# Performance work log

Hardware: AMD Instinct MI355X
Metric: run time of the kernel (lower is better)

The kernel has to match this reference:

```python
import jax, jax.numpy as jnp
import numpy as np

B, C, H, W = 8, 512, 64, 64
INTER = 64


def setup_inputs() -> dict:
    key = jax.random.key(0)
    ks = jax.random.split(key, 9)
    s_in = 1.0 / np.sqrt(C)
    return {
        "query": jax.random.normal(ks[0], (B, C, H, W), jnp.float32),
        "key_t": jax.random.normal(ks[1], (B, C, H, W), jnp.float32),
        "value": jax.random.normal(ks[2], (B, C, H, W), jnp.float32),
        # 1x1 conv weights (squeezed to [out, in]) and biases
        "Wq": jax.random.uniform(ks[3], (INTER, C), jnp.float32, -s_in, s_in),
        "bq": jax.random.uniform(ks[4], (INTER,), jnp.float32, -s_in, s_in),
        "Wk": jax.random.uniform(ks[5], (INTER, C), jnp.float32, -s_in, s_in),
        "bk": jax.random.uniform(ks[6], (INTER,), jnp.float32, -s_in, s_in),
        "Wv": jax.random.uniform(ks[7], (C, C), jnp.float32, -s_in, s_in),
        "bv": jax.random.uniform(ks[8], (C,), jnp.float32, -s_in, s_in),
        "gamma": jnp.full((1,), 0.5, jnp.float32),  # nonzero so attention path is exercised
    }


def reference(query, key_t, value, Wq, bq, Wk, bk, Wv, bv, gamma):
    # 1x1 convs = per-pixel channel matmuls
    pq = jnp.einsum('bchw,oc->bohw', query, Wq) + bq[None, :, None, None]   # [B,INTER,H,W]
    pk = jnp.einsum('bchw,oc->bohw', key_t, Wk) + bk[None, :, None, None]   # [B,INTER,H,W]
    pv = jnp.einsum('bchw,oc->bohw', value, Wv) + bv[None, :, None, None]   # [B,C,H,W]

    # column (height-axis) energies with -inf diagonal, row (width-axis) energies
    eH = jnp.einsum('bchw,bcgw->bhwg', pq, pk)                              # [B,H,W,H]
    eH = jnp.where(jnp.eye(H, dtype=bool)[:, None, :], -jnp.inf, eH)
    eW = jnp.einsum('bchw,bchf->bhwf', pq, pk)                              # [B,H,W,W]

    att = jax.nn.softmax(jnp.concatenate([eH, eW], axis=-1), axis=-1)      # [B,H,W,H+W]
    attH, attW = att[..., :H], att[..., H:]

    out = jnp.einsum('bcgw,bhwg->bchw', pv, attH) \
        + jnp.einsum('bchf,bhwf->bchw', pv, attW)
    return gamma[0] * out + value
```

## Files before the change

### kernel.cpp

```cpp
#include <hip/hip_runtime.h>
#include <hip/hip_bf16.h>

typedef __hip_bfloat16 bf16;
typedef __bf16 v8bf __attribute__((ext_vector_type(8)));
typedef float v4f __attribute__((ext_vector_type(4)));

#define NB 8
#define NC 512
#define NH 64
#define NW 64
#define NHW 4096
#define NI 64

__device__ __forceinline__ float b2f(bf16 x) { return __bfloat162float(x); }
__device__ __forceinline__ bf16  f2b(float x) { return __float2bfloat16(x); }

__global__ __launch_bounds__(256) void prep_kernel(const float* __restrict__ value,
                                                   const float* __restrict__ Wv,
                                                   bf16* __restrict__ vT,
                                                   bf16* __restrict__ Wb) {
  int t = threadIdx.x;
  if (blockIdx.x < 4096) {
    __shared__ float s[64][65];
    int i = blockIdx.x;
    int b = i >> 9, rem = i & 511;
    int c0 = (rem >> 6) * 64, px0 = (rem & 63) * 64;
    int lane = t & 63, row4 = t >> 6;
    const float* vp = value + (size_t)b * NC * NHW;
    for (int r = row4; r < 64; r += 4)
      s[r][lane] = vp[(size_t)(c0 + r) * NHW + px0 + lane];
    __syncthreads();
    bf16* op = vT + (size_t)b * NHW * NC;
    for (int r = row4; r < 64; r += 4)
      op[(size_t)(px0 + r) * NC + c0 + lane] = f2b(s[lane][r]);
  } else {
    size_t idx = (size_t)(blockIdx.x - 4096) * 1024 + t * 4;
    float4 w = *(const float4*)&Wv[idx];
    union { __bf16 h[4]; uint2 u; } pk;
    pk.h[0] = (__bf16)w.x; pk.h[1] = (__bf16)w.y;
    pk.h[2] = (__bf16)w.z; pk.h[3] = (__bf16)w.w;
    *(uint2*)&Wb[idx] = pk.u;
  }
}

__global__ __launch_bounds__(256) void gemm_nt(const bf16* __restrict__ Wb,
                                               const bf16* __restrict__ vT,
                                               const float* __restrict__ bias,
                                               bf16* __restrict__ out) {
  __shared__ __align__(16) __bf16 As[128 * 72];
  __shared__ __align__(16) __bf16 Bs[128 * 72];
  int t = threadIdx.x;
  int b = blockIdx.x >> 5, pxt = blockIdx.x & 31;
  int px0 = pxt * 128, o0 = blockIdx.y * 128;
  int wave = t >> 6, lane = t & 63;
  int wm = (wave >> 1) * 64, wn = (wave & 1) * 64;
  int row16 = lane & 15, quad = lane >> 4;
  v4f acc[4][4] = {};
  const bf16* Bp = vT + ((size_t)b * NHW + px0) * NC;
  for (int k0 = 0; k0 < NC; k0 += 64) {
#pragma unroll
    for (int ii = 0; ii < 4; ++ii) {
      int i = t + ii * 256;
      int m = i >> 3, ch = i & 7;
      *(uint4*)&As[m * 72 + ch * 8] = *(const uint4*)&Wb[(size_t)(o0 + m) * NC + k0 + ch * 8];
      *(uint4*)&Bs[m * 72 + ch * 8] = *(const uint4*)&Bp[(size_t)m * NC + k0 + ch * 8];
    }
    __syncthreads();
#pragma unroll
    for (int ks = 0; ks < 2; ++ks) {
      v8bf af[4], bf[4];
#pragma unroll
      for (int i = 0; i < 4; ++i) {
        af[i] = *(const v8bf*)&As[(wm + i * 16 + row16) * 72 + ks * 32 + quad * 8];
        bf[i] = *(const v8bf*)&Bs[(wn + i * 16 + row16) * 72 + ks * 32 + quad * 8];
      }
#pragma unroll
      for (int mi = 0; mi < 4; ++mi)
#pragma unroll
        for (int ni = 0; ni < 4; ++ni)
          acc[mi][ni] = __builtin_amdgcn_mfma_f32_16x16x32_bf16(af[mi], bf[ni],
                                                                acc[mi][ni], 0, 0, 0);
    }
    __syncthreads();
  }
#pragma unroll
  for (int mi = 0; mi < 4; ++mi)
#pragma unroll
    for (int r = 0; r < 4; ++r) {
      int m = wm + mi * 16 + quad * 4 + r;
      float bi = bias[o0 + m];
      bf16* orow = out + (size_t)(b * NC + o0 + m) * NHW + px0 + wn + row16;
#pragma unroll
      for (int ni = 0; ni < 4; ++ni)
        orow[ni * 16] = f2b(acc[mi][ni][r] + bi);
    }
}

__global__ __launch_bounds__(256) void proj64(const float* __restrict__ X0,
                                              const float* __restrict__ W0,
                                              const float* __restrict__ b0,
                                              bf16* __restrict__ o0p,
                                              const float* __restrict__ X1,
                                              const float* __restrict__ W1,
                                              const float* __restrict__ b1,
                                              bf16* __restrict__ o1p) {
  __shared__ __align__(16) __bf16 As[64 * 72];
  __shared__ __align__(16) __bf16 Bs[128 * 72];
  const float* X = (blockIdx.z == 0) ? X0 : X1;
  const float* Wm = (blockIdx.z == 0) ? W0 : W1;
  const float* bias = (blockIdx.z == 0) ? b0 : b1;
  bf16* out = (blockIdx.z == 0) ? o0p : o1p;
  int t = threadIdx.x;
  int b = blockIdx.x >> 5, nt = blockIdx.x & 31;
  int px0 = nt * 128;
  int wave = t >> 6, lane = t & 63;
  int wm = (wave >> 1) * 32, wn = (wave & 1) * 64;
  int row16 = lane & 15, quad = lane >> 4;
  v4f acc[2][4] = {};
  const float* Xb = X + (size_t)b * NC * NHW + px0;
  for (int k0 = 0; k0 < NC; k0 += 64) {
#pragma unroll
    for (int ii = 0; ii < 4; ++ii) {
      int f = t + ii * 256;
      int m = f >> 4, c4 = (f & 15) * 4;
      float4 w = *(const float4*)&Wm[(size_t)m * NC + k0 + c4];
      union { __bf16 h[4]; uint2 u; } pk;
      pk.h[0] = (__bf16)w.x; pk.h[1] = (__bf16)w.y;
      pk.h[2] = (__bf16)w.z; pk.h[3] = (__bf16)w.w;
      *(uint2*)&As[m * 72 + c4] = pk.u;
    }
#pragma unroll
    for (int r = 0; r < 2; ++r) {
      int idx = r * 256 + t;
      int ch4 = (idx >> 5) * 4, px4 = (idx & 31) * 4;
      float vv[4][4];
#pragma unroll
      for (int j = 0; j < 4; ++j)
        *(float4*)vv[j] = *(const float4*)&Xb[(size_t)(k0 + ch4 + j) * NHW + px4];
#pragma unroll
      for (int i = 0; i < 4; ++i) {
        union { __bf16 h[4]; uint2 u; } pk;
#pragma unroll
        for (int j = 0; j < 4; ++j) pk.h[j] = (__bf16)vv[j][i];
        int px = px4 + i;
        int boff = px * 144 + ((ch4 * 2) ^ (((px >> 2) & 7) << 4));
        *(uint2*)((char*)Bs + boff) = pk.u;
      }
    }
    __syncthreads();
#pragma unroll
    for (int ks = 0; ks < 2; ++ks) {
      v8bf af[2], bf[4];
#pragma unroll
      for (int i = 0; i < 2; ++i)
        af[i] = *(const v8bf*)&As[(wm + i * 16 + row16) * 72 + ks * 32 + quad * 8];
#pragma unroll
      for (int i = 0; i < 4; ++i) {
        int px = wn + i * 16 + row16;
        int boff = px * 144 + ((ks * 64 + quad * 16) ^ (((px >> 2) & 7) << 4));
        bf[i] = *(const v8bf*)((const char*)Bs + boff);
      }
#pragma unroll
      for (int mi = 0; mi < 2; ++mi)
#pragma unroll
        for (int ni = 0; ni < 4; ++ni)
          acc[mi][ni] = __builtin_amdgcn_mfma_f32_16x16x32_bf16(af[mi], bf[ni],
                                                                acc[mi][ni], 0, 0, 0);
    }
    __syncthreads();
  }
#pragma unroll
  for (int mi = 0; mi < 2; ++mi)
#pragma unroll
    for (int r = 0; r < 4; ++r) {
      int m = wm + mi * 16 + quad * 4 + r;
      float bi = bias[m];
      bf16* orow = out + (size_t)(b * NI + m) * NHW + px0 + wn + row16;
#pragma unroll
      for (int ni = 0; ni < 4; ++ni)
        orow[ni * 16] = f2b(acc[mi][ni][r] + bi);
    }
}

__device__ __forceinline__ void tile_mac(const float (*As)[68], const float (*Bs)[68],
                                         float acc[4][4], int tc, int tr) {
#pragma unroll 16
  for (int k = 0; k < 64; ++k) {
    float a0 = As[k][tc], a1 = As[k][tc + 1], a2 = As[k][tc + 2], a3 = As[k][tc + 3];
    float b0 = Bs[k][tr], b1 = Bs[k][tr + 1], b2 = Bs[k][tr + 2], b3 = Bs[k][tr + 3];
    acc[0][0] += a0 * b0; acc[0][1] += a0 * b1; acc[0][2] += a0 * b2; acc[0][3] += a0 * b3;
    acc[1][0] += a1 * b0; acc[1][1] += a1 * b1; acc[1][2] += a1 * b2; acc[1][3] += a1 * b3;
    acc[2][0] += a2 * b0; acc[2][1] += a2 * b1; acc[2][2] += a2 * b2; acc[2][3] += a2 * b3;
    acc[3][0] += a3 * b0; acc[3][1] += a3 * b1; acc[3][2] += a3 * b2; acc[3][3] += a3 * b3;
  }
}

__global__ __launch_bounds__(256) void score_kernel(const bf16* __restrict__ pq,
                                                    const bf16* __restrict__ pk,
                                                    float* __restrict__ att) {
  __shared__ float As[64][68];
  __shared__ float Bs[64][68];
  int t = threadIdx.x, lane = t & 63, row4 = t >> 6;
  int b = blockIdx.x >> 6, q = blockIdx.x & 63;
  bool isH = (blockIdx.y == 0);
  const bf16* pqb = pq + (size_t)b * NI * NHW;
  const bf16* pkb = pk + (size_t)b * NI * NHW;
  for (int o = row4; o < 64; o += 4) {
    size_t base = (size_t)o * NHW;
    if (isH) {
      As[o][lane] = b2f(pqb[base + (size_t)lane * NW + q]);
      Bs[o][lane] = b2f(pkb[base + (size_t)lane * NW + q]);
    } else {
      As[o][lane] = b2f(pqb[base + (size_t)q * NW + lane]);
      Bs[o][lane] = b2f(pkb[base + (size_t)q * NW + lane]);
    }
  }
  __syncthreads();
  int tc = (t & 15) * 4, tr = (t >> 4) * 4;
  float acc[4][4] = {};
  tile_mac(As, Bs, acc, tc, tr);
#pragma unroll
  for (int i = 0; i < 4; ++i)
#pragma unroll
    for (int j = 0; j < 4; ++j) {
      if (isH) {
        int h = tc + i, g = tr + j;
        float v = (h == g) ? -1e30f : acc[i][j];
        att[((size_t)(b * 64 + h) * 64 + q) * 128 + g] = v;
      } else {
        int w = tc + i, f = tr + j;
        att[((size_t)(b * 64 + q) * 64 + w) * 128 + 64 + f] = acc[i][j];
      }
    }
}

__global__ __launch_bounds__(256) void softmax_kernel(float* __restrict__ att) {
  int wave = threadIdx.x >> 6, lane = threadIdx.x & 63;
  int p = blockIdx.x * 4 + wave;
  float* row = att + (size_t)p * 128;
  float v0 = row[lane], v1 = row[lane + 64];
  float m = fmaxf(v0, v1);
#pragma unroll
  for (int off = 32; off; off >>= 1) m = fmaxf(m, __shfl_xor(m, off));
  float e0 = __expf(v0 - m), e1 = __expf(v1 - m);
  float s = e0 + e1;
#pragma unroll
  for (int off = 32; off; off >>= 1) s += __shfl_xor(s, off);
  float inv = 1.0f / s;
  bf16* rb = (bf16*)row;
  rb[lane] = f2b(e0 * inv);
  rb[lane + 64] = f2b(e1 * inv);
}

__global__ __launch_bounds__(256) void transpose_kernel(const bf16* __restrict__ in,
                                                        bf16* __restrict__ out) {
  __shared__ float s[64][65];
  int lane = threadIdx.x & 63, row4 = threadIdx.x >> 6;
  const bf16* ip = in + (size_t)blockIdx.x * 4096;
  bf16* op = out + (size_t)blockIdx.x * 4096;
  for (int r = row4; r < 64; r += 4) s[r][lane] = b2f(ip[r * 64 + lane]);
  __syncthreads();
  for (int r = row4; r < 64; r += 4) op[r * 64 + lane] = f2b(s[lane][r]);
}

__global__ __launch_bounds__(256) void apply_mfma(const bf16* pva,
                                                  const bf16* __restrict__ attb,
                                                  bf16* outp, int mode, int strided) {
  __shared__ __align__(16) __bf16 As[128 * 72];
  __shared__ __align__(16) __bf16 Bs[64 * 72];
  int t = threadIdx.x;
  int b = blockIdx.x >> 6, q = blockIdx.x & 63;
  int c0 = blockIdx.y * 128;
  int wave = t >> 6, lane = t & 63;
  int row16 = lane & 15, quad = lane >> 4;
#pragma unroll
  for (int ii = 0; ii < 4; ++ii) {
    int i = t + ii * 256;
    int m = i >> 3, ch = i & 7;
    if (!strided) {
      *(uint4*)&As[m * 72 + ch * 8] =
          *(const uint4*)&pva[((size_t)(b * NC + c0 + m) * 64 + q) * 64 + ch * 8];
    } else {
      union { __bf16 h[8]; uint4 u; } pk;
#pragma unroll
      for (int j = 0; j < 8; ++j)
        pk.h[j] = (__bf16)b2f(pva[(size_t)(b * NC + c0 + m) * 4096 +
                                  (size_t)(ch * 8 + j) * 64 + q]);
      *(uint4*)&As[m * 72 + ch * 8] = pk.u;
    }
  }
#pragma unroll
  for (int ii = 0; ii < 2; ++ii) {
    int i = t + ii * 256;
    int n = i >> 3, ch = i & 7;
    const bf16* src = (mode == 0)
        ? &attb[((size_t)(b * 64 + n) * 64 + q) * 256 + ch * 8]
        : &attb[((size_t)(b * 64 + q) * 64 + n) * 256 + 64 + ch * 8];
    *(uint4*)&Bs[n * 72 + ch * 8] = *(const uint4*)src;
  }
  __syncthreads();
  v4f acc[2][4] = {};
#pragma unroll
  for (int ks = 0; ks < 2; ++ks) {
    v8bf af[2], bfr[4];
#pragma unroll
    for (int mi = 0; mi < 2; ++mi)
      af[mi] = *(const v8bf*)&As[(wave * 32 + mi * 16 + row16) * 72 + ks * 32 + quad * 8];
#pragma unroll
    for (int ni = 0; ni < 4; ++ni)
      bfr[ni] = *(const v8bf*)&Bs[(ni * 16 + row16) * 72 + ks * 32 + quad * 8];
#pragma unroll
    for (int mi = 0; mi < 2; ++mi)
#pragma unroll
      for (int ni = 0; ni < 4; ++ni)
        acc[mi][ni] = __builtin_amdgcn_mfma_f32_16x16x32_bf16(af[mi], bfr[ni],
                                                              acc[mi][ni], 0, 0, 0);
  }
#pragma unroll
  for (int mi = 0; mi < 2; ++mi)
#pragma unroll
    for (int ni = 0; ni < 4; ++ni)
#pragma unroll
      for (int r = 0; r < 4; ++r) {
        int c = c0 + wave * 32 + mi * 16 + quad * 4 + r;
        int hw = row16 + ni * 16;
        outp[((size_t)(b * NC + c) * 64 + q) * 64 + hw] = f2b(acc[mi][ni][r]);
      }
}

__global__ __launch_bounds__(256) void combine_kernel(const bf16* __restrict__ t1,
                                                      const bf16* t2,
                                                      const float* __restrict__ value,
                                                      const float* __restrict__ gamma,
                                                      float* __restrict__ out) {
  __shared__ float s[64][65];
  int lane = threadIdx.x & 63, row4 = threadIdx.x >> 6;
  size_t bc = blockIdx.x;
  const bf16* t1p = t1 + bc * 4096;
  for (int r = row4; r < 64; r += 4) s[r][lane] = b2f(t1p[r * 64 + lane]);
  __syncthreads();
  float g = gamma[0];
  const bf16* t2p = t2 + bc * 4096;
  const float* vp = value + bc * 4096;
  float* op = out + bc * 4096;
  for (int r = row4; r < 64; r += 4)
    op[r * 64 + lane] = g * (s[lane][r] + b2f(t2p[r * 64 + lane])) + vp[r * 64 + lane];
}

extern "C" void kernel_launch(void* const* d_in, const int* in_sizes, int n_in,
                              void* d_out, int out_size, void* d_ws, size_t ws_size,
                              hipStream_t stream) {
  const float* query = (const float*)d_in[0];
  const float* key_t = (const float*)d_in[1];
  const float* value = (const float*)d_in[2];
  const float* Wq    = (const float*)d_in[3];
  const float* bq    = (const float*)d_in[4];
  const float* Wk    = (const float*)d_in[5];
  const float* bk    = (const float*)d_in[6];
  const float* Wv    = (const float*)d_in[7];
  const float* bv    = (const float*)d_in[8];
  const float* gamma = (const float*)d_in[9];
  float* out = (float*)d_out;

  char* ws = (char*)d_ws;
  bool full = ws_size >= (120ull << 20);
  bf16*  pq  = (bf16*)(ws);
  bf16*  Wb  = (bf16*)(ws);
  bf16*  pk  = (bf16*)(ws + (4ull << 20));
  float* att = (float*)(ws + (8ull << 20));
  bf16*  attb = (bf16*)att;
  bf16*  pv  = (bf16*)(ws + (24ull << 20));
  bf16*  pvT = (bf16*)(ws + (56ull << 20));
  bf16*  vT  = (bf16*)(ws + ((full ? 88ull : 56ull) << 20));
  bf16*  t1  = vT;
  bf16*  t2  = pv;

  dim3 blk(256);
  prep_kernel<<<4096 + 256, blk, 0, stream>>>(value, Wv, vT, Wb);
  gemm_nt<<<dim3(NB * 32, 4), blk, 0, stream>>>(Wb, vT, bv, pv);
  if (full) transpose_kernel<<<NB * NC, blk, 0, stream>>>(pv, pvT);
  proj64<<<dim3(NB * 32, 1, 2), blk, 0, stream>>>(
      query, Wq, bq, pq, key_t, Wk, bk, pk);
  score_kernel<<<dim3(NB * 64, 2), blk, 0, stream>>>(pq, pk, att);
  softmax_kernel<<<NB * NHW / 4, blk, 0, stream>>>(att);
  apply_mfma<<<dim3(NB * 64, 4), blk, 0, stream>>>(
      full ? pvT : pv, attb, t1, 0, full ? 0 : 1);
  apply_mfma<<<dim3(NB * 64, 4), blk, 0, stream>>>(pv, attb, t2, 1, 0);
  combine_kernel<<<NB * NC, blk, 0, stream>>>(t1, t2, value, gamma, out);
}
```

Before: 365.3 us.

## Double-buffer projection input via direct global-to-LDS loads, pre-convert Wq/Wk

Replaces the Q/K 1x1-conv projection kernel with one that streams fp32 activation tiles straight into LDS using global_load_lds, double-buffered so the next channel slice loads while MFMAs run on the current one. The LDS layout uses a rotated column swizzle to reduce bank conflicts. Wq and Wk are now converted to bf16 once in the prep kernel and read directly from global memory as MFMA A-fragments, instead of being converted and staged per block. Values are converted fp32->bf16 when read from LDS, which adds scalar LDS reads and conversions. The extra weight buffer reuses workspace space later overwritten by the attention scores.

```diff
diff --git a/kernel.cpp b/kernel.cpp
--- a/kernel.cpp
+++ b/kernel.cpp
@@ -17,8 +17,12 @@
 
 __global__ __launch_bounds__(256) void prep_kernel(const float* __restrict__ value,
                                                    const float* __restrict__ Wv,
+                                                   const float* __restrict__ Wq,
+                                                   const float* __restrict__ Wk,
                                                    bf16* __restrict__ vT,
-                                                   bf16* __restrict__ Wb) {
+                                                   bf16* __restrict__ Wb,
+                                                   bf16* __restrict__ Wqb,
+                                                   bf16* __restrict__ Wkb) {
   int t = threadIdx.x;
   if (blockIdx.x < 4096) {
     __shared__ float s[64][65];
@@ -34,12 +38,17 @@
     for (int r = row4; r < 64; r += 4)
       op[(size_t)(px0 + r) * NC + c0 + lane] = f2b(s[lane][r]);
   } else {
-    size_t idx = (size_t)(blockIdx.x - 4096) * 1024 + t * 4;
-    float4 w = *(const float4*)&Wv[idx];
+    int wb = blockIdx.x - 4096;
+    const float* src; bf16* dst; int lb;
+    if (wb < 256)      { src = Wv; dst = Wb;  lb = wb; }
+    else if (wb < 288) { src = Wq; dst = Wqb; lb = wb - 256; }
+    else               { src = Wk; dst = Wkb; lb = wb - 288; }
+    size_t idx = (size_t)lb * 1024 + t * 4;
+    float4 w = *(const float4*)&src[idx];
     union { __bf16 h[4]; uint2 u; } pk;
     pk.h[0] = (__bf16)w.x; pk.h[1] = (__bf16)w.y;
     pk.h[2] = (__bf16)w.z; pk.h[3] = (__bf16)w.w;
-    *(uint2*)&Wb[idx] = pk.u;
+    *(uint2*)&dst[idx] = pk.u;
   }
 }
 
@@ -96,78 +105,91 @@
     }
 }
 
-__global__ __launch_bounds__(256) void proj64(const float* __restrict__ X0,
-                                              const float* __restrict__ W0,
-                                              const float* __restrict__ b0,
-                                              bf16* __restrict__ o0p,
-                                              const float* __restrict__ X1,
-                                              const float* __restrict__ W1,
-                                              const float* __restrict__ b1,
-                                              bf16* __restrict__ o1p) {
-  __shared__ __align__(16) __bf16 As[64 * 72];
-  __shared__ __align__(16) __bf16 Bs[128 * 72];
-  const float* X = (blockIdx.z == 0) ? X0 : X1;
-  const float* Wm = (blockIdx.z == 0) ? W0 : W1;
+__global__ __launch_bounds__(256) void proj_lds(const float* __restrict__ X0,
+                                                const bf16* __restrict__ Wb0,
+                                                const float* __restrict__ b0,
+                                                bf16* __restrict__ o0p,
+                                                const float* __restrict__ X1,
+                                                const bf16* __restrict__ Wb1,
+                                                const float* __restrict__ b1,
+                                                bf16* __restrict__ o1p) {
+  __shared__ __align__(16) float Xs[2][64][128];
+  const float* X    = (blockIdx.z == 0) ? X0 : X1;
+  const bf16*  Wmb  = (blockIdx.z == 0) ? Wb0 : Wb1;
   const float* bias = (blockIdx.z == 0) ? b0 : b1;
-  bf16* out = (blockIdx.z == 0) ? o0p : o1p;
+  bf16* out         = (blockIdx.z == 0) ? o0p : o1p;
   int t = threadIdx.x;
   int b = blockIdx.x >> 5, nt = blockIdx.x & 31;
   int px0 = nt * 128;
   int wave = t >> 6, lane = t & 63;
   int wm = (wave >> 1) * 32, wn = (wave & 1) * 64;
   int row16 = lane & 15, quad = lane >> 4;
+  const float* Xb = X + (size_t)b * NC * NHW + px0;
+  int lhalf = lane >> 5;
+  int lcol  = (lane & 31) << 4;
   v4f acc[2][4] = {};
-  const float* Xb = X + (size_t)b * NC * NHW + px0;
-  for (int k0 = 0; k0 < NC; k0 += 64) {
-#pragma unroll
-    for (int ii = 0; ii < 4; ++ii) {
-      int f = t + ii * 256;
-      int m = f >> 4, c4 = (f & 15) * 4;
-      float4 w = *(const float4*)&Wm[(size_t)m * NC + k0 + c4];
-      union { __bf16 h[4]; uint2 u; } pk;
-      pk.h[0] = (__bf16)w.x; pk.h[1] = (__bf16)w.y;
-      pk.h[2] = (__bf16)w.z; pk.h[3] = (__bf16)w.w;
-      *(uint2*)&As[m * 72 + c4] = pk.u;
-    }
-#pragma unroll
-    for (int r = 0; r < 2; ++r) {
-      int idx = r * 256 + t;
-      int ch4 = (idx >> 5) * 4, px4 = (idx & 31) * 4;
-      float vv[4][4];
-#pragma unroll
-      for (int j = 0; j < 4; ++j)
-        *(float4*)vv[j] = *(const float4*)&Xb[(size_t)(k0 + ch4 + j) * NHW + px4];
-#pragma unroll
-      for (int i = 0; i < 4; ++i) {
-        union { __bf16 h[4]; uint2 u; } pk;
-#pragma unroll
-        for (int j = 0; j < 4; ++j) pk.h[j] = (__bf16)vv[j][i];
-        int px = px4 + i;
-        int boff = px * 144 + ((ch4 * 2) ^ (((px >> 2) & 7) << 4));
-        *(uint2*)((char*)Bs + boff) = pk.u;
+#pragma unroll
+  for (int i = 0; i < 8; ++i) {
+    int c  = (wave << 4) + (i << 1);
+    int ch = c + lhalf;
+    int pxl = ((lcol - (((ch >> 3) & 7) << 6)) & 511) >> 2;
+    const float* g = Xb + (size_t)ch * NHW + pxl;
+    __builtin_amdgcn_global_load_lds(
+        (const __attribute__((address_space(1))) void*)g,
+        (__attribute__((address_space(3))) void*)&Xs[0][c][0], 16, 0, 0);
+  }
+#pragma unroll
+  for (int k = 0; k < 8; ++k) {
+    int k0 = k * 64;
+    v8bf af[2][2];
+#pragma unroll
+    for (int ks = 0; ks < 2; ++ks)
+#pragma unroll
+      for (int i = 0; i < 2; ++i)
+        af[ks][i] = *(const v8bf*)&Wmb[(size_t)(wm + i * 16 + row16) * NC +
+                                       k0 + ks * 32 + quad * 8];
+    __builtin_amdgcn_sched_barrier(0);
+    if (k != 7) {
+      int kn = k0 + 64;
+#pragma unroll
+      for (int i = 0; i < 8; ++i) {
+        int c  = (wave << 4) + (i << 1);
+        int ch = c + lhalf;
+        int pxl = ((lcol - (((ch >> 3) & 7) << 6)) & 511) >> 2;
+        const float* g = Xb + (size_t)(kn + ch) * NHW + pxl;
+        __builtin_amdgcn_global_load_lds(
+            (const __attribute__((address_space(1))) void*)g,
+            (__attribute__((address_space(3))) void*)&Xs[(k + 1) & 1][c][0], 16, 0, 0);
       }
-    }
-    __syncthreads();
+      asm volatile("s_waitcnt vmcnt(8)" ::: "memory");
+    } else {
+      asm volatile("s_waitcnt vmcnt(0)" ::: "memory");
+    }
+    __builtin_amdgcn_s_barrier();
+    const float(*Xc)[128] = Xs[k & 1];
 #pragma unroll
     for (int ks = 0; ks < 2; ++ks) {
-      v8bf af[2], bf[4];
-#pragma unroll
-      for (int i = 0; i < 2; ++i)
-        af[i] = *(const v8bf*)&As[(wm + i * 16 + row16) * 72 + ks * 32 + quad * 8];
+      int rot = (ks * 4 + quad) << 6;
+      v8bf bfr[4];
 #pragma unroll
       for (int i = 0; i < 4; ++i) {
         int px = wn + i * 16 + row16;
-        int boff = px * 144 + ((ks * 64 + quad * 16) ^ (((px >> 2) & 7) << 4));
-        bf[i] = *(const v8bf*)((const char*)Bs + boff);
+        int colb = ((px << 2) + rot) & 511;
+        const char* base = (const char*)&Xc[ks * 32 + quad * 8][0] + colb;
+        union { __bf16 h[8]; v8bf v; } pk;
+#pragma unroll
+        for (int j = 0; j < 8; ++j)
+          pk.h[j] = (__bf16)(*(const float*)(base + j * 512));
+        bfr[i] = pk.v;
       }
 #pragma unroll
       for (int mi = 0; mi < 2; ++mi)
 #pragma unroll
         for (int ni = 0; ni < 4; ++ni)
-          acc[mi][ni] = __builtin_amdgcn_mfma_f32_16x16x32_bf16(af[mi], bf[ni],
+          acc[mi][ni] = __builtin_amdgcn_mfma_f32_16x16x32_bf16(af[ks][mi], bfr[ni],
                                                                 acc[mi][ni], 0, 0, 0);
     }
-    __syncthreads();
+    __builtin_amdgcn_s_barrier();
   }
 #pragma unroll
   for (int mi = 0; mi < 2; ++mi)
@@ -368,6 +390,8 @@
   bf16*  Wb  = (bf16*)(ws);
   bf16*  pk  = (bf16*)(ws + (4ull << 20));
   float* att = (float*)(ws + (8ull << 20));
+  bf16*  Wqb = (bf16*)(ws + (8ull << 20));
+  bf16*  Wkb = Wqb + 64 * 512;
   bf16*  attb = (bf16*)att;
   bf16*  pv  = (bf16*)(ws + (24ull << 20));
   bf16*  pvT = (bf16*)(ws + (56ull << 20));
@@ -376,11 +400,12 @@
   bf16*  t2  = pv;
 
   dim3 blk(256);
-  prep_kernel<<<4096 + 256, blk, 0, stream>>>(value, Wv, vT, Wb);
+  prep_kernel<<<4096 + 256 + 64, blk, 0, stream>>>(value, Wv, Wq, Wk,
+                                                   vT, Wb, Wqb, Wkb);
   gemm_nt<<<dim3(NB * 32, 4), blk, 0, stream>>>(Wb, vT, bv, pv);
   if (full) transpose_kernel<<<NB * NC, blk, 0, stream>>>(pv, pvT);
-  proj64<<<dim3(NB * 32, 1, 2), blk, 0, stream>>>(
-      query, Wq, bq, pq, key_t, Wk, bk, pk);
+  proj_lds<<<dim3(NB * 32, 1, 2), blk, 0, stream>>>(
+      query, Wqb, bq, pq, key_t, Wkb, bk, pk);
   score_kernel<<<dim3(NB * 64, 2), blk, 0, stream>>>(pq, pk, att);
   softmax_kernel<<<NB * NHW / 4, blk, 0, stream>>>(att);
   apply_mfma<<<dim3(NB * 64, 4), blk, 0, stream>>>(
```

New measurement: 357.7 us. -2.1%, faster.
